# Kernel optimization log

Hardware: AMD Instinct MI355X
Metric: run time of the kernel (lower is better)

## Reference

```python
import jax, jax.numpy as jnp
import numpy as np

H = 16
D_MODEL = 1024
D_K = D_MODEL // H
NEG = -1e9


def setup_inputs() -> dict:
    key = jax.random.key(0)
    ks = jax.random.split(key, 12)
    B, S = 2, 2048
    inp = {
        "query": jax.random.normal(ks[0], (B, S, D_MODEL), jnp.float32),
        "key": jax.random.normal(ks[1], (B, S, D_MODEL), jnp.float32),
        "value": jax.random.normal(ks[2], (B, S, D_MODEL), jnp.float32),
        "mask": jnp.ones((B, 1, S), jnp.int32),
    }
    s = 1.0 / np.sqrt(D_MODEL)
    for i, nm in enumerate(["Wq", "Wk", "Wv", "Wo"]):
        inp[nm] = jax.random.normal(ks[3 + i], (D_MODEL, D_MODEL), jnp.float32) * s
        inp["b" + nm[1]] = jax.random.normal(ks[7 + i], (D_MODEL,), jnp.float32) * s
    return inp


def _split_heads(x):
    B, S, _ = x.shape
    return x.reshape(B, S, H, D_K).transpose(0, 2, 1, 3)  # [B,H,S,Dk]


def reference(query, key, value, mask, Wq, bq, Wk, bk, Wv, bv, Wo, bo):
    q = _split_heads(query @ Wq + bq)
    k = _split_heads(key @ Wk + bk)
    v = _split_heads(value @ Wv + bv)
    scores = jnp.einsum("bhqd,bhkd->bhqk", q, k) / jnp.sqrt(jnp.float32(D_K))
    # mask [B,1,Sk] -> broadcast as [B,1,1,Sk]
    scores = jnp.where(mask[:, None, :, :] == 0, NEG, scores)
    attn = jax.nn.softmax(scores, axis=-1)  # dropout is identity in eval mode
    out = jnp.einsum("bhqk,bhkd->bhqd", attn, v)
    B, _, Sq, _ = out.shape
    out = out.transpose(0, 2, 1, 3).reshape(B, Sq, H * D_K)
    return out @ Wo + bo
```

## Files before the change

### kernel.cpp

```cpp
#include <hip/hip_runtime.h>
#include <hip/hip_bf16.h>

typedef __attribute__((ext_vector_type(8))) short short8;
typedef __attribute__((ext_vector_type(4))) float float4v;
typedef __attribute__((ext_vector_type(2))) unsigned int uint2v;
typedef __hip_bfloat16 bf16;

#define MFMA16(a, b, c) __builtin_amdgcn_mfma_f32_16x16x32_bf16((a), (b), (c), 0, 0, 0)

static __device__ __forceinline__ short8 load8(const bf16* p) {
    return *reinterpret_cast<const short8*>(p);
}
static __device__ __forceinline__ unsigned short bfu(float x) {
    union { bf16 b; unsigned short u; } c; c.b = __float2bfloat16(x); return c.u;
}
static __device__ __forceinline__ unsigned pack2(float lo, float hi) {
    return ((unsigned)bfu(hi) << 16) | bfu(lo);
}
static __device__ __forceinline__ short bf_bits(float x) {
    union { bf16 b; short u; } c; c.b = __float2bfloat16(x); return c.u;
}
static __device__ __forceinline__ short8 cvt8(float4 a, float4 b) {
    short8 r;
    r[0] = bf_bits(a.x); r[1] = bf_bits(a.y); r[2] = bf_bits(a.z); r[3] = bf_bits(a.w);
    r[4] = bf_bits(b.x); r[5] = bf_bits(b.y); r[6] = bf_bits(b.z); r[7] = bf_bits(b.w);
    return r;
}

typedef const __attribute__((address_space(1))) unsigned int* gp1;
typedef __attribute__((address_space(3))) unsigned int* lp3;
static __device__ __forceinline__ void async16(const void* g, void* l) {
    __builtin_amdgcn_global_load_lds((gp1)g, (lp3)l, 16, 0, 0);
}

__global__ __launch_bounds__(256) void transpose_qkv(
    const float* __restrict__ Wq, const float* __restrict__ Wk,
    const float* __restrict__ Wv, bf16* __restrict__ out_base)
{
    __shared__ bf16 tile[64][65];
    const float* in = (blockIdx.z == 0) ? Wq : (blockIdx.z == 1) ? Wk : Wv;
    bf16* out = out_base + (size_t)blockIdx.z * 1048576;
    int tx = threadIdx.x, ty = threadIdx.y;
    int bx = blockIdx.x * 64, by = blockIdx.y * 64;
    for (int i = ty; i < 64; i += 4)
        tile[i][tx] = __float2bfloat16(in[(size_t)(by + i) * 1024 + bx + tx]);
    __syncthreads();
    for (int i = ty; i < 64; i += 4)
        out[(size_t)(bx + i) * 1024 + by + tx] = tile[tx][i];
}

__global__ __launch_bounds__(256) void transpose_one(
    const float* __restrict__ in, bf16* __restrict__ out)
{
    __shared__ bf16 tile[64][65];
    int tx = threadIdx.x, ty = threadIdx.y;
    int bx = blockIdx.x * 64, by = blockIdx.y * 64;
    for (int i = ty; i < 64; i += 4)
        tile[i][tx] = __float2bfloat16(in[(size_t)(by + i) * 1024 + bx + tx]);
    __syncthreads();
    for (int i = ty; i < 64; i += 4)
        out[(size_t)(bx + i) * 1024 + by + tx] = tile[tx][i];
}

__global__ __launch_bounds__(256, 3) void qkv_gemm(
    const float* __restrict__ Xq, const float* __restrict__ Xk,
    const float* __restrict__ Xv, const bf16* __restrict__ Wt_all,
    const float* __restrict__ bq, const float* __restrict__ bk,
    const float* __restrict__ bv,
    bf16* __restrict__ outq, bf16* __restrict__ outk, bf16* __restrict__ outv)
{
    __shared__ float As[128 * 64];
    __shared__ bf16  Bs[128 * 64];

    int wg = blockIdx.x;
    int xcd = wg & 7;
    int jj = wg >> 3;
    int grp = xcd * 12 + (jj >> 3);
    int z = grp >> 5;
    int m_blk = grp & 31;
    int n_blk = jj & 7;

    const float* X    = (z == 0) ? Xq : (z == 1) ? Xk : Xv;
    const float* bias = (z == 0) ? bq : (z == 1) ? bk : bv;
    const bf16*  Wt   = Wt_all + (size_t)z * 1048576;
    bf16*        out  = (z == 0) ? outq : (z == 1) ? outk : outv;
    bool vmode = (z == 2);

    int tid = threadIdx.x;
    int w = tid >> 6, lane = tid & 63, l16 = lane & 15, quad = lane >> 4;
    int m_base = m_blk * 128, n_base = n_blk * 128;

    int r4 = lane >> 4, s16 = lane & 15;
    int r8 = lane >> 3, s8 = lane & 7;
    const float* Asrc0 = X + (size_t)(m_base + w * 32 + r4) * 1024 + ((s16 ^ r4) << 2);
    const float* Asrc1 = X + (size_t)(m_base + w * 32 + r4) * 1024 + ((s16 ^ (4 + r4)) << 2);
    const bf16*  Bsrc  = Wt + (size_t)(n_base + w * 32 + r8) * 1024 + ((s8 ^ r8) << 3);

    int wm = (w & 1) * 64, wn = (w >> 1) * 64;
    int sw = l16 & 7;

    float4v zero = {0.f, 0.f, 0.f, 0.f};
    float4v acc[4][4];
    #pragma unroll
    for (int mi = 0; mi < 4; ++mi)
        #pragma unroll
        for (int nj = 0; nj < 4; ++nj) acc[mi][nj] = zero;

    for (int it = 0; it < 16; ++it) {
        int kt = it * 64;
        #pragma unroll
        for (int p = 0; p < 8; ++p) {
            const float* s = ((p & 1) ? Asrc1 : Asrc0) + (size_t)p * 4096 + kt;
            async16(s, (char*)As + (w * 32 + p * 4) * 256);
        }
        #pragma unroll
        for (int p = 0; p < 4; ++p)
            async16(Bsrc + (size_t)p * 8192 + kt, (char*)Bs + (w * 32 + p * 8) * 128);
        __syncthreads();

        #pragma unroll
        for (int kk = 0; kk < 2; ++kk) {
            short8 af[4], bfr[4];
            #pragma unroll
            for (int mi = 0; mi < 4; ++mi) {
                const float* rp = As + (wm + mi * 16 + l16) * 64;
                float4 f0 = *(const float4*)(rp + (((kk * 8 + quad * 2)     ^ sw) << 2));
                float4 f1 = *(const float4*)(rp + (((kk * 8 + quad * 2 + 1) ^ sw) << 2));
                af[mi] = cvt8(f0, f1);
            }
            #pragma unroll
            for (int nj = 0; nj < 4; ++nj) {
                const bf16* rp = Bs + (wn + nj * 16 + l16) * 64;
                bfr[nj] = load8(rp + (((kk * 4 + quad) ^ sw) << 3));
            }
            #pragma unroll
            for (int mi = 0; mi < 4; ++mi)
                #pragma unroll
                for (int nj = 0; nj < 4; ++nj)
                    acc[mi][nj] = MFMA16(af[mi], bfr[nj], acc[mi][nj]);
        }
        __syncthreads();
    }

    float bsv[4];
    #pragma unroll
    for (int nj = 0; nj < 4; ++nj)
        bsv[nj] = bias[n_base + wn + nj * 16 + l16];

    #pragma unroll
    for (int mi = 0; mi < 4; ++mi) {
        #pragma unroll
        for (int nj = 0; nj < 4; ++nj) {
            int n = n_base + wn + nj * 16 + l16;
            int h = n >> 6, dk = n & 63;
            int m0 = m_base + wm + mi * 16 + quad * 4;
            int b = m0 >> 11, s0 = m0 & 2047;
            if (vmode) {
                float v0 = acc[mi][nj][0] + bsv[nj];
                float v1 = acc[mi][nj][1] + bsv[nj];
                float v2 = acc[mi][nj][2] + bsv[nj];
                float v3 = acc[mi][nj][3] + bsv[nj];
                uint2 pv; pv.x = pack2(v0, v1); pv.y = pack2(v2, v3);
                size_t idx = ((size_t)(b * 16 + h) * 64 + dk) * 2048 + s0;
                *reinterpret_cast<uint2*>(out + idx) = pv;
            } else {
                #pragma unroll
                for (int r = 0; r < 4; ++r) {
                    size_t idx = (((size_t)(b * 16 + h) * 2048 + s0 + r) * 64 + dk);
                    out[idx] = __float2bfloat16(acc[mi][nj][r] + bsv[nj]);
                }
            }
        }
    }
}

__global__ __launch_bounds__(256, 2) void out_gemm(
    const bf16* __restrict__ A, const bf16* __restrict__ Wt,
    const float* __restrict__ bias, float* __restrict__ out)
{
    __shared__ bf16 As[128 * 64];
    __shared__ bf16 Bs[64 * 64];

    int wg = blockIdx.x;
    int xcd = wg & 7;
    int jj = wg >> 3;
    int m_blk = xcd * 4 + (jj >> 4);
    int n_blk = jj & 15;

    int tid = threadIdx.x;
    int w = tid >> 6, lane = tid & 63, l16 = lane & 15, quad = lane >> 4;
    int m_base = m_blk * 128, n_base = n_blk * 64;

    int r8 = lane >> 3, s8 = lane & 7;
    const bf16* Asrc = A  + (size_t)(m_base + w * 32 + r8) * 1024 + ((s8 ^ r8) << 3);
    const bf16* Bsrc = Wt + (size_t)(n_base + w * 16 + r8) * 1024 + ((s8 ^ r8) << 3);

    int wm = (w & 1) * 64, wn = (w >> 1) * 32;
    int sw = l16 & 7;

    float4v zero = {0.f, 0.f, 0.f, 0.f};
    float4v acc[4][2];
    #pragma unroll
    for (int mi = 0; mi < 4; ++mi)
        #pragma unroll
        for (int nj = 0; nj < 2; ++nj) acc[mi][nj] = zero;

    for (int it = 0; it < 16; ++it) {
        int kt = it * 64;
        #pragma unroll
        for (int p = 0; p < 4; ++p)
            async16(Asrc + (size_t)p * 8192 + kt, (char*)As + (w * 32 + p * 8) * 128);
        #pragma unroll
        for (int p = 0; p < 2; ++p)
            async16(Bsrc + (size_t)p * 8192 + kt, (char*)Bs + (w * 16 + p * 8) * 128);
        __syncthreads();

        #pragma unroll
        for (int kk = 0; kk < 2; ++kk) {
            short8 af[4], bfr[2];
            #pragma unroll
            for (int mi = 0; mi < 4; ++mi) {
                const bf16* rp = As + (wm + mi * 16 + l16) * 64;
                af[mi] = load8(rp + (((kk * 4 + quad) ^ sw) << 3));
            }
            #pragma unroll
            for (int nj = 0; nj < 2; ++nj) {
                const bf16* rp = Bs + (wn + nj * 16 + l16) * 64;
                bfr[nj] = load8(rp + (((kk * 4 + quad) ^ sw) << 3));
            }
            #pragma unroll
            for (int mi = 0; mi < 4; ++mi)
                #pragma unroll
                for (int nj = 0; nj < 2; ++nj)
                    acc[mi][nj] = MFMA16(af[mi], bfr[nj], acc[mi][nj]);
        }
        __syncthreads();
    }

    float bsv[2];
    #pragma unroll
    for (int nj = 0; nj < 2; ++nj)
        bsv[nj] = bias[n_base + wn + nj * 16 + l16];

    #pragma unroll
    for (int mi = 0; mi < 4; ++mi)
        #pragma unroll
        for (int nj = 0; nj < 2; ++nj) {
            int n = n_base + wn + nj * 16 + l16;
            int m0 = m_base + wm + mi * 16 + quad * 4;
            #pragma unroll
            for (int r = 0; r < 4; ++r)
                out[(size_t)(m0 + r) * 1024 + n] = acc[mi][nj][r] + bsv[nj];
        }
}

__global__ __launch_bounds__(512, 4) void attn_fused(
    const bf16* __restrict__ Qm, const bf16* __restrict__ Km,
    const bf16* __restrict__ Vt, const int* __restrict__ mask,
    bf16* __restrict__ Oout)
{
    __shared__ __align__(16) bf16 Kc[2][64 * 64];
    __shared__ __align__(16) bf16 Vc[2][64 * 64];
    __shared__ unsigned long long maskb[32];

    int tid = threadIdx.x;
    int w = tid >> 6, lane = tid & 63, l16 = lane & 15, quad = lane >> 4;
    int wg = blockIdx.x;
    int xcd = wg & 7;
    int jj = wg >> 3;
    int bh = xcd * 4 + (jj >> 4);
    int qg = jj & 15;
    int b = bh >> 4, h = bh & 15;
    int qt = qg * 8 + w;

    const int* mb = mask + b * 2048;
    #pragma unroll
    for (int i = 0; i < 4; ++i) {
        unsigned long long bal = __ballot(mb[w * 256 + i * 64 + lane] != 0);
        if (lane == 0) maskb[w * 4 + i] = bal;
    }

    const bf16* Qb = Qm + ((size_t)bh * 2048 + (size_t)qt * 16) * 64;
    short8 bQ0 = load8(Qb + l16 * 64 + quad * 8);
    short8 bQ1 = load8(Qb + l16 * 64 + 32 + quad * 8);

    int r8 = lane >> 3, s8 = lane & 7;
    const bf16* Ksrc = Km + (size_t)bh * 131072 + (size_t)(w * 8 + r8) * 64 + ((s8 ^ r8) << 3);
    const bf16* Vsrc = Vt + (size_t)bh * 131072 + (size_t)(w * 8 + r8) * 2048 + ((s8 ^ r8) << 3);

    int sw = l16 & 7;

    float4v zero = {0.f, 0.f, 0.f, 0.f};
    float4v Oacc[4];
    #pragma unroll
    for (int g = 0; g < 4; ++g) Oacc[g] = zero;
    float lsum = 0.f;
    const float C = 0.18033688f;

    async16(Ksrc, (char*)&Kc[0][0] + w * 1024);
    async16(Vsrc, (char*)&Vc[0][0] + w * 1024);
    __syncthreads();

    #pragma unroll 2
    for (int it = 0; it < 32; ++it) {
        int cur = it & 1;
        if (it != 31) {
            async16(Ksrc + (size_t)(it + 1) * 4096, (char*)&Kc[cur ^ 1][0] + w * 1024);
            async16(Vsrc + (size_t)(it + 1) * 64,   (char*)&Vc[cur ^ 1][0] + w * 1024);
        }

        unsigned long long m64 = maskb[it];
        bool full = (m64 == ~0ull);
        const bf16* Kb = &Kc[cur][0];
        const bf16* Vb = &Vc[cur][0];

        float4v S[4];
        #pragma unroll
        for (int kj = 0; kj < 4; ++kj) {
            const bf16* kr = Kb + (kj * 16 + l16) * 64;
            short8 a0 = load8(kr + (((0 + quad) ^ sw) << 3));
            short8 a1 = load8(kr + (((4 + quad) ^ sw) << 3));
            float4v s = MFMA16(a0, bQ0, zero);
            s = MFMA16(a1, bQ1, s);
            S[kj] = s;
        }

        unsigned wlo[4], whi[4];
        #pragma unroll
        for (int kj = 0; kj < 4; ++kj) {
            unsigned m4 = (unsigned)(m64 >> (kj * 16 + quad * 4)) & 0xFu;
            float p[4];
            #pragma unroll
            for (int r = 0; r < 4; ++r)
                p[r] = __builtin_amdgcn_exp2f(S[kj][r] * C);
            if (!full) {
                #pragma unroll
                for (int r = 0; r < 4; ++r)
                    p[r] = ((m4 >> r) & 1u) ? p[r] : 0.f;
            }
            lsum += (p[0] + p[1]) + (p[2] + p[3]);
            wlo[kj] = pack2(p[0], p[1]);
            whi[kj] = pack2(p[2], p[3]);
        }

        short8 ap[2];
        #pragma unroll
        for (int m = 0; m < 2; ++m) {
            uint2v sa = __builtin_amdgcn_permlane32_swap(wlo[2 * m], wlo[2 * m + 1], false, false);
            uint2v qa = __builtin_amdgcn_permlane16_swap(sa[0], sa[1], false, false);
            uint2v sb = __builtin_amdgcn_permlane32_swap(whi[2 * m], whi[2 * m + 1], false, false);
            uint2v qb = __builtin_amdgcn_permlane16_swap(sb[0], sb[1], false, false);
            union { short8 s; unsigned u[4]; } t;
            t.u[0] = qa[0];
            t.u[1] = qb[0];
            t.u[2] = qa[1];
            t.u[3] = qb[1];
            ap[m] = t.s;
        }

        #pragma unroll
        for (int g = 0; g < 4; ++g) {
            const bf16* vr = Vb + (g * 16 + l16) * 64;
            short8 v0 = load8(vr + (((0 + quad) ^ sw) << 3));
            short8 v1 = load8(vr + (((4 + quad) ^ sw) << 3));
            Oacc[g] = MFMA16(ap[0], v0, Oacc[g]);
            Oacc[g] = MFMA16(ap[1], v1, Oacc[g]);
        }

        __syncthreads();
    }

    float ls = lsum;
    ls += __shfl_xor(ls, 16, 64);
    ls += __shfl_xor(ls, 32, 64);
    #pragma unroll
    for (int r = 0; r < 4; ++r) {
        float linv = 1.f / __shfl(ls, quad * 4 + r, 64);
        int srow = qt * 16 + quad * 4 + r;
        size_t base = ((size_t)b * 2048 + srow) * 1024 + h * 64;
        #pragma unroll
        for (int g = 0; g < 4; ++g)
            Oout[base + g * 16 + l16] = __float2bfloat16(Oacc[g][r] * linv);
    }
}

extern "C" void kernel_launch(void* const* d_in, const int* in_sizes, int n_in,
                              void* d_out, int out_size, void* d_ws, size_t ws_size,
                              hipStream_t stream) {
    const float* query = (const float*)d_in[0];
    const float* key   = (const float*)d_in[1];
    const float* value = (const float*)d_in[2];
    const int*   mask  = (const int*)d_in[3];
    const float* Wq = (const float*)d_in[4];
    const float* bq = (const float*)d_in[5];
    const float* Wk = (const float*)d_in[6];
    const float* bk = (const float*)d_in[7];
    const float* Wv = (const float*)d_in[8];
    const float* bv = (const float*)d_in[9];
    const float* Wo = (const float*)d_in[10];
    const float* bo = (const float*)d_in[11];

    char* ws = (char*)d_ws;
    const size_t MB = 1024 * 1024;
    bf16* vb     = (bf16*)ws;
    bf16* Wt_all = (bf16*)(ws + 8 * MB);
    bf16* aout   = (bf16*)(ws + 8 * MB);
    bf16* WtO    = (bf16*)ws;
    bf16* qb     = (bf16*)d_out;
    bf16* kb     = (bf16*)((char*)d_out + 8 * MB);
    float* out   = (float*)d_out;

    transpose_qkv<<<dim3(16, 16, 3), dim3(64, 4), 0, stream>>>(Wq, Wk, Wv, Wt_all);

    qkv_gemm<<<dim3(768), 256, 0, stream>>>(
        query, key, value, Wt_all, bq, bk, bv, qb, kb, vb);

    attn_fused<<<dim3(512), 512, 0, stream>>>(qb, kb, vb, mask, aout);

    transpose_one<<<dim3(16, 16), dim3(64, 4), 0, stream>>>(Wo, WtO);

    out_gemm<<<dim3(512), 256, 0, stream>>>(aout, WtO, bo, out);
}
```

Measured before the change: 243.7 us.

## Double-buffer shared memory tiles in QKV and output projection GEMMs

Both projection GEMMs now use two shared-memory buffers so the async global-to-LDS copy of the next K tile is issued before computing on the current tile, with one barrier per iteration. The QKV GEMM halves its K tile to 32 to keep LDS usage within the same footprint, which changes the swizzle and load mapping. This aims to hide global load latency behind MFMA work, at the cost of more loop iterations in qkv_gemm and twice the LDS in out_gemm, which may reduce occupancy.

```diff
diff --git a/kernel.cpp b/kernel.cpp
--- a/kernel.cpp
+++ b/kernel.cpp
@@ -69,8 +69,8 @@
     const float* __restrict__ bv,
     bf16* __restrict__ outq, bf16* __restrict__ outk, bf16* __restrict__ outv)
 {
-    __shared__ float As[128 * 64];
-    __shared__ bf16  Bs[128 * 64];
+    __shared__ float As[2][128 * 32];
+    __shared__ bf16  Bs[2][128 * 32];
 
     int wg = blockIdx.x;
     int xcd = wg & 7;
@@ -90,14 +90,13 @@
     int w = tid >> 6, lane = tid & 63, l16 = lane & 15, quad = lane >> 4;
     int m_base = m_blk * 128, n_base = n_blk * 128;
 
-    int r4 = lane >> 4, s16 = lane & 15;
-    int r8 = lane >> 3, s8 = lane & 7;
-    const float* Asrc0 = X + (size_t)(m_base + w * 32 + r4) * 1024 + ((s16 ^ r4) << 2);
-    const float* Asrc1 = X + (size_t)(m_base + w * 32 + r4) * 1024 + ((s16 ^ (4 + r4)) << 2);
-    const bf16*  Bsrc  = Wt + (size_t)(n_base + w * 32 + r8) * 1024 + ((s8 ^ r8) << 3);
+    int r8  = lane >> 3, s8 = lane & 7;
+    int r16 = lane >> 2, s4 = lane & 3;
+    const float* Asrc = X  + (size_t)(m_base + w * 32 + r8) * 1024 + ((s8 ^ r8) << 2);
+    const bf16*  Bsrc = Wt + (size_t)(n_base + w * 32 + r16) * 1024 + ((s4 ^ (r16 & 3)) << 3);
 
     int wm = (w & 1) * 64, wn = (w >> 1) * 64;
-    int sw = l16 & 7;
+    int sw = l16 & 7, sw3 = l16 & 3;
 
     float4v zero = {0.f, 0.f, 0.f, 0.f};
     float4v acc[4][4];
@@ -106,39 +105,49 @@
         #pragma unroll
         for (int nj = 0; nj < 4; ++nj) acc[mi][nj] = zero;
 
-    for (int it = 0; it < 16; ++it) {
-        int kt = it * 64;
-        #pragma unroll
-        for (int p = 0; p < 8; ++p) {
-            const float* s = ((p & 1) ? Asrc1 : Asrc0) + (size_t)p * 4096 + kt;
-            async16(s, (char*)As + (w * 32 + p * 4) * 256);
-        }
-        #pragma unroll
-        for (int p = 0; p < 4; ++p)
-            async16(Bsrc + (size_t)p * 8192 + kt, (char*)Bs + (w * 32 + p * 8) * 128);
-        __syncthreads();
-
-        #pragma unroll
-        for (int kk = 0; kk < 2; ++kk) {
-            short8 af[4], bfr[4];
-            #pragma unroll
-            for (int mi = 0; mi < 4; ++mi) {
-                const float* rp = As + (wm + mi * 16 + l16) * 64;
-                float4 f0 = *(const float4*)(rp + (((kk * 8 + quad * 2)     ^ sw) << 2));
-                float4 f1 = *(const float4*)(rp + (((kk * 8 + quad * 2 + 1) ^ sw) << 2));
-                af[mi] = cvt8(f0, f1);
-            }
-            #pragma unroll
-            for (int nj = 0; nj < 4; ++nj) {
-                const bf16* rp = Bs + (wn + nj * 16 + l16) * 64;
-                bfr[nj] = load8(rp + (((kk * 4 + quad) ^ sw) << 3));
-            }
-            #pragma unroll
-            for (int mi = 0; mi < 4; ++mi)
-                #pragma unroll
-                for (int nj = 0; nj < 4; ++nj)
-                    acc[mi][nj] = MFMA16(af[mi], bfr[nj], acc[mi][nj]);
-        }
+    #pragma unroll
+    for (int p = 0; p < 4; ++p)
+        async16(Asrc + (size_t)p * 8192, (char*)&As[0][0] + (w * 32 + p * 8) * 128);
+    #pragma unroll
+    for (int p = 0; p < 2; ++p)
+        async16(Bsrc + (size_t)p * 16384, (char*)&Bs[0][0] + (w * 32 + p * 16) * 64);
+    __syncthreads();
+
+    for (int it = 0; it < 32; ++it) {
+        int cur = it & 1;
+        if (it != 31) {
+            int kt = (it + 1) * 32;
+            #pragma unroll
+            for (int p = 0; p < 4; ++p)
+                async16(Asrc + (size_t)p * 8192 + kt,
+                        (char*)&As[cur ^ 1][0] + (w * 32 + p * 8) * 128);
+            #pragma unroll
+            for (int p = 0; p < 2; ++p)
+                async16(Bsrc + (size_t)p * 16384 + kt,
+                        (char*)&Bs[cur ^ 1][0] + (w * 32 + p * 16) * 64);
+        }
+
+        const float* Ab = &As[cur][0];
+        const bf16*  Bb = &Bs[cur][0];
+        short8 af[4], bfr[4];
+        #pragma unroll
+        for (int mi = 0; mi < 4; ++mi) {
+            const float* rp = Ab + (wm + mi * 16 + l16) * 32;
+            float4 f0 = *(const float4*)(rp + (((quad * 2)     ^ sw) << 2));
+            float4 f1 = *(const float4*)(rp + (((quad * 2 + 1) ^ sw) << 2));
+            af[mi] = cvt8(f0, f1);
+        }
+        #pragma unroll
+        for (int nj = 0; nj < 4; ++nj) {
+            const bf16* rp = Bb + (wn + nj * 16 + l16) * 32;
+            bfr[nj] = load8(rp + ((quad ^ sw3) << 3));
+        }
+        #pragma unroll
+        for (int mi = 0; mi < 4; ++mi)
+            #pragma unroll
+            for (int nj = 0; nj < 4; ++nj)
+                acc[mi][nj] = MFMA16(af[mi], bfr[nj], acc[mi][nj]);
+
         __syncthreads();
     }
 
@@ -178,8 +187,8 @@
     const bf16* __restrict__ A, const bf16* __restrict__ Wt,
     const float* __restrict__ bias, float* __restrict__ out)
 {
-    __shared__ bf16 As[128 * 64];
-    __shared__ bf16 Bs[64 * 64];
+    __shared__ bf16 As[2][128 * 64];
+    __shared__ bf16 Bs[2][64 * 64];
 
     int wg = blockIdx.x;
     int xcd = wg & 7;
@@ -205,27 +214,41 @@
         #pragma unroll
         for (int nj = 0; nj < 2; ++nj) acc[mi][nj] = zero;
 
+    #pragma unroll
+    for (int p = 0; p < 4; ++p)
+        async16(Asrc + (size_t)p * 8192, (char*)&As[0][0] + (w * 32 + p * 8) * 128);
+    #pragma unroll
+    for (int p = 0; p < 2; ++p)
+        async16(Bsrc + (size_t)p * 8192, (char*)&Bs[0][0] + (w * 16 + p * 8) * 128);
+    __syncthreads();
+
     for (int it = 0; it < 16; ++it) {
-        int kt = it * 64;
-        #pragma unroll
-        for (int p = 0; p < 4; ++p)
-            async16(Asrc + (size_t)p * 8192 + kt, (char*)As + (w * 32 + p * 8) * 128);
-        #pragma unroll
-        for (int p = 0; p < 2; ++p)
-            async16(Bsrc + (size_t)p * 8192 + kt, (char*)Bs + (w * 16 + p * 8) * 128);
-        __syncthreads();
-
+        int cur = it & 1;
+        if (it != 15) {
+            int kt = (it + 1) * 64;
+            #pragma unroll
+            for (int p = 0; p < 4; ++p)
+                async16(Asrc + (size_t)p * 8192 + kt,
+                        (char*)&As[cur ^ 1][0] + (w * 32 + p * 8) * 128);
+            #pragma unroll
+            for (int p = 0; p < 2; ++p)
+                async16(Bsrc + (size_t)p * 8192 + kt,
+                        (char*)&Bs[cur ^ 1][0] + (w * 16 + p * 8) * 128);
+        }
+
+        const bf16* Ab = &As[cur][0];
+        const bf16* Bb = &Bs[cur][0];
         #pragma unroll
         for (int kk = 0; kk < 2; ++kk) {
             short8 af[4], bfr[2];
             #pragma unroll
             for (int mi = 0; mi < 4; ++mi) {
-                const bf16* rp = As + (wm + mi * 16 + l16) * 64;
+                const bf16* rp = Ab + (wm + mi * 16 + l16) * 64;
                 af[mi] = load8(rp + (((kk * 4 + quad) ^ sw) << 3));
             }
             #pragma unroll
             for (int nj = 0; nj < 2; ++nj) {
-                const bf16* rp = Bs + (wn + nj * 16 + l16) * 64;
+                const bf16* rp = Bb + (wn + nj * 16 + l16) * 64;
                 bfr[nj] = load8(rp + (((kk * 4 + quad) ^ sw) << 3));
             }
             #pragma unroll
```

After: 264.7 us. 8.6% more time.
